# Performance work log

Hardware: AMD Instinct MI355X
Metric: run time of the kernel (lower is better)

## Reference

```python
import jax, jax.numpy as jnp
import numpy as np

jax.config.update("jax_enable_x64", True)  # int64 quantized math requires x64

Q = 23  # q23 fixed-point fraction bits


def _shift_linear(x, w, shift):
    """int64 GEMM with per-tensor arithmetic-shift rescale: (x @ w.T) >> shift.
    Models int64_bmm_broadcast with x_rescale=weight_rescale=1, res_rescale=shift
    (quotient part; the remainder is only used for the zk proof, not the output)."""
    acc = jnp.einsum('td,fd->tf', x, w.astype(jnp.int64))  # [T, out]
    return jnp.right_shift(acc, shift)  # arithmetic shift on signed int64


def silu_q23(r):
    """Fixed-point SiLU: s = round(silu(r / 2^Q) * 2^Q), int64 in/out."""
    xf = r.astype(jnp.float64) / float(1 << Q)
    y = xf * jax.nn.sigmoid(xf)
    return jnp.round(y * float(1 << Q)).astype(jnp.int64)


def setup_inputs() -> dict:
    key = jax.random.key(0)
    k1, k2, k3, k4 = jax.random.split(key, 4)
    T, D, F = 8192, 2048, 1408  # tokens, dim, inter_dim
    # q23 activations, centered so silu exercises both branches
    x = jax.random.randint(k1, (T, D), 0, 1 << 20, dtype=jnp.int64) - (1 << 19)
    w1 = (jax.random.randint(k2, (F, D), 0, 256, dtype=jnp.int32) - 128)
    w3 = (jax.random.randint(k3, (F, D), 0, 256, dtype=jnp.int32) - 128)
    w2 = (jax.random.randint(k4, (D, F), 0, 256, dtype=jnp.int32) - 128)
    return {"x": x, "w1": w1, "w2": w2, "w3": w3,
            "scale1": 23, "scale2": 23, "scale3": 23}


def reference(x, w1, w2, w3, scale1, scale2, scale3):
    # r1 = w1(x):  int64 GEMM + shift rescale
    r1 = _shift_linear(x, w1, scale1)            # [T, F] q23
    s1 = silu_q23(r1)                            # [T, F] q23
    r2 = _shift_linear(x, w3, scale3)            # [T, F] q23
    gate = jnp.right_shift(s1 * r2, Q)           # q23 * q23 >> 23 -> q23
    q = _shift_linear(gate, w2, scale2)          # [T, D]
    return q
```

## Files before the change

### kernel.cpp

```cpp
#include <hip/hip_runtime.h>
#include <math.h>

typedef int i32x4 __attribute__((ext_vector_type(4)));
typedef int i32x16 __attribute__((ext_vector_type(16)));

#define NT_M 128
#define NT_D 32
#define NT_F 22
#define DDIM 2048
#define FDIM 1408

#define OFFSWZ(r, k) (((r) << 6) + ((((((k) >> 4)) + ((r) >> 1)) & 3) << 4) + ((k) & 15))

__device__ __forceinline__ void gld_lds16(const void* gp, void* lp) {
  auto* l = reinterpret_cast<unsigned int __attribute__((address_space(3)))*>(
      (unsigned int)(unsigned long long)(lp));
  const auto* g = reinterpret_cast<const unsigned int __attribute__((address_space(1)))*>(
      (unsigned long long)(gp));
  __builtin_amdgcn_global_load_lds(g, l, 16, 0, 0);
}

__device__ __forceinline__ i32x16 zero16() {
  i32x16 z;
#pragma unroll
  for (int e = 0; e < 16; ++e) z[e] = 0;
  return z;
}

__global__ __launch_bounds__(256) void pack_x_kernel(const int* __restrict__ x,
                                                     signed char* __restrict__ XD) {
  const int tk = blockIdx.x;
  const int tm = blockIdx.y;
  const int tid = threadIdx.x;
  signed char* tile = XD + (size_t)(tm * NT_D + tk) * 3 * 4096;
  const int* base = x + (size_t)tm * 64 * DDIM + tk * 64;
#pragma unroll
  for (int i = 0; i < 4; ++i) {
    const int gi = i * 256 + tid;
    const int row = gi >> 4;
    const int k4 = (gi & 15) << 2;
    const i32x4 v = *(const i32x4*)(base + (size_t)row * DDIM + k4);
    unsigned p0 = 0, p1 = 0, p2 = 0;
#pragma unroll
    for (int j = 0; j < 4; ++j) {
      const int val = v[j];
      const int b0 = (int)(signed char)(val & 0xff);
      const int c = (val - b0) >> 8;
      const int b1 = (int)(signed char)(c & 0xff);
      const int b2 = (c - b1) >> 8;
      p0 |= ((unsigned)(val & 0xff)) << (8 * j);
      p1 |= ((unsigned)(c & 0xff)) << (8 * j);
      p2 |= ((unsigned)(b2 & 0xff)) << (8 * j);
    }
    const int off = OFFSWZ(row, k4);
    *(unsigned*)(tile + off) = p0;
    *(unsigned*)(tile + 4096 + off) = p1;
    *(unsigned*)(tile + 8192 + off) = p2;
  }
}

__global__ __launch_bounds__(256) void pack_w_kernel(const int* __restrict__ w1,
                                                     const int* __restrict__ w3,
                                                     const int* __restrict__ w2,
                                                     signed char* __restrict__ W1T,
                                                     signed char* __restrict__ W3T,
                                                     signed char* __restrict__ W2T) {
  const int which = blockIdx.y;
  const int t = blockIdx.x;
  const int tid = threadIdx.x;
  const int* src;
  signed char* dst;
  int rowstride, nk;
  if (which == 0)      { src = w1; dst = W1T; rowstride = DDIM; nk = NT_D; }
  else if (which == 1) { src = w3; dst = W3T; rowstride = DDIM; nk = NT_D; }
  else                 { src = w2; dst = W2T; rowstride = FDIM; nk = NT_F; }
  const int tr = t / nk, tk = t % nk;
  signed char* tile = dst + (size_t)t * 4096;
  const int* base = src + (size_t)tr * 64 * rowstride + tk * 64;
#pragma unroll
  for (int i = 0; i < 4; ++i) {
    const int gi = i * 256 + tid;
    const int row = gi >> 4;
    const int k4 = (gi & 15) << 2;
    const i32x4 v = *(const i32x4*)(base + (size_t)row * rowstride + k4);
    const unsigned p = ((unsigned)(v[0] & 0xff)) | ((unsigned)(v[1] & 0xff) << 8) |
                       ((unsigned)(v[2] & 0xff) << 16) | ((unsigned)(v[3] & 0xff) << 24);
    *(unsigned*)(tile + OFFSWZ(row, k4)) = p;
  }
}

__global__ __launch_bounds__(256, 2) void gemm1_kernel(
    const signed char* __restrict__ XD, const signed char* __restrict__ W1T,
    const signed char* __restrict__ W3T, signed char* __restrict__ GATE,
    const int* __restrict__ scale1p, const int* __restrict__ scale3p) {
  __shared__ __align__(16) signed char lds[40960];
  const int tid = threadIdx.x;
  const int wv = tid >> 6;
  const int lane = tid & 63;
  const int r32 = lane & 31;
  const int g = lane >> 5;
  const int tf = blockIdx.x;
  const int tm = blockIdx.y;
  const int wm = wv >> 1, wn = wv & 1;

  i32x16 acc10 = zero16(), acc11 = zero16(), acc12 = zero16();
  i32x16 acc30 = zero16(), acc31 = zero16(), acc32 = zero16();

  const signed char* srcAbase = XD + (size_t)tm * NT_D * 3 * 4096;
  const signed char* srcB1base = W1T + (size_t)tf * NT_D * 4096;
  const signed char* srcB3base = W3T + (size_t)tf * NT_D * 4096;

  auto stage = [&](int kt, int b) {
#pragma unroll
    for (int j = 0; j < 3; ++j) {
      const int ch = wv * 3 + j;
      gld_lds16(srcAbase + (size_t)kt * 12288 + ch * 1024 + lane * 16,
                lds + b * 12288 + ch * 1024);
    }
#pragma unroll
    for (int j = 0; j < 2; ++j) {
      const int ch = wv * 2 + j;
      const signed char* s = (ch < 4) ? srcB1base + (size_t)kt * 4096 + ch * 1024
                                      : srcB3base + (size_t)kt * 4096 + (ch - 4) * 1024;
      gld_lds16(s + lane * 16, lds + 24576 + b * 8192 + ch * 1024);
    }
  };

  stage(0, 0);

  const int arow = wm * 32 + r32;
  const int brow = wn * 32 + r32;
  const int aoffbase = arow * 64;
  const int boffbase = brow * 64;
  const int ash = arow >> 1;
  const int bsh = brow >> 1;

  for (int kt = 0; kt < NT_D; ++kt) {
    const int b = kt & 1;
    __syncthreads();
    if (kt + 1 < NT_D) stage(kt + 1, b ^ 1);
    const signed char* A = lds + b * 12288;
    const signed char* B = lds + 24576 + b * 8192;
#pragma unroll
    for (int kk = 0; kk < 2; ++kk) {
      const int ks = kk * 2 + g;
      const int sa = (ks + ash) & 3;
      const int sb = (ks + bsh) & 3;
      const i32x4 a0 = *(const i32x4*)(A + aoffbase + sa * 16);
      const i32x4 a1 = *(const i32x4*)(A + 4096 + aoffbase + sa * 16);
      const i32x4 a2 = *(const i32x4*)(A + 8192 + aoffbase + sa * 16);
      const i32x4 bb1 = *(const i32x4*)(B + boffbase + sb * 16);
      const i32x4 bb3 = *(const i32x4*)(B + 4096 + boffbase + sb * 16);
      acc10 = __builtin_amdgcn_mfma_i32_32x32x32_i8(a0, bb1, acc10, 0, 0, 0);
      acc11 = __builtin_amdgcn_mfma_i32_32x32x32_i8(a1, bb1, acc11, 0, 0, 0);
      acc12 = __builtin_amdgcn_mfma_i32_32x32x32_i8(a2, bb1, acc12, 0, 0, 0);
      acc30 = __builtin_amdgcn_mfma_i32_32x32x32_i8(a0, bb3, acc30, 0, 0, 0);
      acc31 = __builtin_amdgcn_mfma_i32_32x32x32_i8(a1, bb3, acc31, 0, 0, 0);
      acc32 = __builtin_amdgcn_mfma_i32_32x32x32_i8(a2, bb3, acc32, 0, 0, 0);
    }
  }

  const int s1v = scale1p[0];
  const int s3v = scale3p[0];
  signed char* gt = GATE + (size_t)(tm * NT_F + tf) * 4096;
  const int colf = wn * 32 + r32;
  const double QINV = 1.0 / 8388608.0;
#pragma unroll
  for (int e = 0; e < 16; ++e) {
    const int rowe = (e & 3) + 8 * (e >> 2) + 4 * g;
    const int ml = wm * 32 + rowe;
    const long long av1 =
        (long long)acc10[e] + ((long long)acc11[e] << 8) + ((long long)acc12[e] << 16);
    const long long r1 = av1 >> s1v;
    const long long av3 =
        (long long)acc30[e] + ((long long)acc31[e] << 8) + ((long long)acc32[e] << 16);
    const long long r2 = av3 >> s3v;
    const double xf = (double)r1 * QINV;
    const double t = exp(-fabs(xf));
    const double sg = (xf >= 0.0) ? (1.0 / (1.0 + t)) : (t / (1.0 + t));
    const long long s1q = (long long)rint((double)r1 * sg);
    const long long gv = (s1q * r2) >> 23;
    gt[OFFSWZ(ml, colf)] = (signed char)gv;
  }
}

__global__ __launch_bounds__(256, 2) void gemm2_kernel(
    const signed char* __restrict__ GATE, const signed char* __restrict__ W2T,
    int* __restrict__ out, const int* __restrict__ scale2p) {
  __shared__ __align__(16) signed char lds[32768];
  const int tid = threadIdx.x;
  const int wv = tid >> 6;
  const int lane = tid & 63;
  const int r32 = lane & 31;
  const int g = lane >> 5;
  const int tn = blockIdx.x;
  const int tm = blockIdx.y;
  const int wm = wv >> 1, wn = wv & 1;

  i32x16 acc00 = zero16(), acc01 = zero16(), acc10 = zero16(), acc11 = zero16();

  auto stage = [&](int kt, int b) {
#pragma unroll
    for (int j = 0; j < 2; ++j) {
      const int ch = wv * 2 + j;
      gld_lds16(GATE + ((size_t)((tm * 2 + (ch >> 2)) * NT_F + kt)) * 4096 + (ch & 3) * 1024 +
                    lane * 16,
                lds + b * 8192 + ch * 1024);
    }
#pragma unroll
    for (int j = 0; j < 2; ++j) {
      const int ch = wv * 2 + j;
      gld_lds16(W2T + ((size_t)((tn * 2 + (ch >> 2)) * NT_F + kt)) * 4096 + (ch & 3) * 1024 +
                    lane * 16,
                lds + 16384 + b * 8192 + ch * 1024);
    }
  };

  stage(0, 0);
  const int r0 = r32, r1r = 32 + r32;
  const int s0b = r0 >> 1, s1b = r1r >> 1;

  for (int kt = 0; kt < NT_F; ++kt) {
    const int b = kt & 1;
    __syncthreads();
    if (kt + 1 < NT_F) stage(kt + 1, b ^ 1);
    const signed char* A = lds + b * 8192 + wm * 4096;
    const signed char* B = lds + 16384 + b * 8192 + wn * 4096;
#pragma unroll
    for (int kk = 0; kk < 2; ++kk) {
      const int ks = kk * 2 + g;
      const int sa0 = (ks + s0b) & 3;
      const int sa1 = (ks + s1b) & 3;
      const i32x4 a0 = *(const i32x4*)(A + r0 * 64 + sa0 * 16);
      const i32x4 a1 = *(const i32x4*)(A + r1r * 64 + sa1 * 16);
      const i32x4 b0 = *(const i32x4*)(B + r0 * 64 + sa0 * 16);
      const i32x4 b1 = *(const i32x4*)(B + r1r * 64 + sa1 * 16);
      acc00 = __builtin_amdgcn_mfma_i32_32x32x32_i8(a0, b0, acc00, 0, 0, 0);
      acc01 = __builtin_amdgcn_mfma_i32_32x32x32_i8(a0, b1, acc01, 0, 0, 0);
      acc10 = __builtin_amdgcn_mfma_i32_32x32x32_i8(a1, b0, acc10, 0, 0, 0);
      acc11 = __builtin_amdgcn_mfma_i32_32x32x32_i8(a1, b1, acc11, 0, 0, 0);
    }
  }

  const int s2v = scale2p[0];
  int* obase = out + (size_t)(tm * 128 + wm * 64) * DDIM + tn * 128 + wn * 64;
#pragma unroll
  for (int e = 0; e < 16; ++e) {
    const int rowe = (e & 3) + 8 * (e >> 2) + 4 * g;
    obase[(size_t)rowe * DDIM + r32] = acc00[e] >> s2v;
    obase[(size_t)rowe * DDIM + 32 + r32] = acc01[e] >> s2v;
    obase[(size_t)(rowe + 32) * DDIM + r32] = acc10[e] >> s2v;
    obase[(size_t)(rowe + 32) * DDIM + 32 + r32] = acc11[e] >> s2v;
  }
}

extern "C" void kernel_launch(void* const* d_in, const int* in_sizes, int n_in,
                              void* d_out, int out_size, void* d_ws, size_t ws_size,
                              hipStream_t stream) {
  if (n_in < 7) return;
  const int* x = (const int*)d_in[0];
  const int* w1 = (const int*)d_in[1];
  const int* w2 = (const int*)d_in[2];
  const int* w3 = (const int*)d_in[3];
  const int* s1 = (const int*)d_in[4];
  const int* s2 = (const int*)d_in[5];
  const int* s3 = (const int*)d_in[6];
  signed char* ws = (signed char*)d_ws;
  int* out = (int*)d_out;

  const size_t XD_OFF = 0;
  const size_t XD_SZ = (size_t)NT_M * NT_D * 3 * 4096;
  const size_t WT_SZ = (size_t)NT_F * NT_D * 4096;
  const size_t W1_OFF = XD_OFF + XD_SZ;
  const size_t W3_OFF = W1_OFF + WT_SZ;
  const size_t W2_OFF = W3_OFF + WT_SZ;
  const size_t GATE_OFF = W2_OFF + WT_SZ;
  const size_t GATE_SZ = (size_t)NT_M * NT_F * 4096;
  if (ws_size < GATE_OFF + GATE_SZ) return;

  pack_x_kernel<<<dim3(NT_D, NT_M), 256, 0, stream>>>(x, ws + XD_OFF);
  pack_w_kernel<<<dim3(704, 3), 256, 0, stream>>>(w1, w3, w2, ws + W1_OFF, ws + W3_OFF,
                                                  ws + W2_OFF);
  gemm1_kernel<<<dim3(NT_F, NT_M), 256, 0, stream>>>(ws + XD_OFF, ws + W1_OFF, ws + W3_OFF,
                                                     ws + GATE_OFF, s1, s3);
  gemm2_kernel<<<dim3(DDIM / 128, NT_M / 2), 256, 0, stream>>>(ws + GATE_OFF, ws + W2_OFF,
                                                               out, s2);
}
```

Baseline: 207.2 us.

## Enlarge gemm1 M-tile to 128 rows with 8 waves and remap block order

gemm1 now uses 512-thread blocks covering two 64-row M tiles, so each staged W1/W3 tile is reused across twice as many rows and B traffic is halved. LDS grows to 64KB per block. Both GEMMs also switch to a 1D grid with block index swizzling, grouping 8 M-tiles across the XCDs to improve L2 locality. The risks are lower occupancy from the larger LDS footprint and the launch_bounds(512,4) register pressure.

```diff
diff --git a/kernel.cpp b/kernel.cpp
--- a/kernel.cpp
+++ b/kernel.cpp
@@ -89,58 +89,63 @@
   }
 }
 
-__global__ __launch_bounds__(256, 2) void gemm1_kernel(
+__global__ __launch_bounds__(512, 4) void gemm1_kernel(
     const signed char* __restrict__ XD, const signed char* __restrict__ W1T,
     const signed char* __restrict__ W3T, signed char* __restrict__ GATE,
     const int* __restrict__ scale1p, const int* __restrict__ scale3p) {
-  __shared__ __align__(16) signed char lds[40960];
+  __shared__ __align__(16) signed char lds[65536];
   const int tid = threadIdx.x;
   const int wv = tid >> 6;
   const int lane = tid & 63;
   const int r32 = lane & 31;
   const int g = lane >> 5;
-  const int tf = blockIdx.x;
-  const int tm = blockIdx.y;
+  const int bi = blockIdx.x;
+  const int c = bi & 7;
+  const int q = bi >> 3;
+  const int tm2 = (q / 22) * 8 + c;
+  const int tf = q % 22;
   const int wm = wv >> 1, wn = wv & 1;
 
   i32x16 acc10 = zero16(), acc11 = zero16(), acc12 = zero16();
   i32x16 acc30 = zero16(), acc31 = zero16(), acc32 = zero16();
 
-  const signed char* srcAbase = XD + (size_t)tm * NT_D * 3 * 4096;
   const signed char* srcB1base = W1T + (size_t)tf * NT_D * 4096;
   const signed char* srcB3base = W3T + (size_t)tf * NT_D * 4096;
 
   auto stage = [&](int kt, int b) {
+    const int sub = wv >> 2;
 #pragma unroll
     for (int j = 0; j < 3; ++j) {
       const int ch = wv * 3 + j;
-      gld_lds16(srcAbase + (size_t)kt * 12288 + ch * 1024 + lane * 16,
-                lds + b * 12288 + ch * 1024);
-    }
-#pragma unroll
-    for (int j = 0; j < 2; ++j) {
-      const int ch = wv * 2 + j;
+      const int chs = ch - sub * 12;
+      gld_lds16(XD + (size_t)((tm2 * 2 + sub) * NT_D + kt) * 12288 + chs * 1024 + lane * 16,
+                lds + b * 24576 + ch * 1024);
+    }
+    {
+      const int ch = wv;
       const signed char* s = (ch < 4) ? srcB1base + (size_t)kt * 4096 + ch * 1024
                                       : srcB3base + (size_t)kt * 4096 + (ch - 4) * 1024;
-      gld_lds16(s + lane * 16, lds + 24576 + b * 8192 + ch * 1024);
+      gld_lds16(s + lane * 16, lds + 49152 + b * 8192 + ch * 1024);
     }
   };
 
   stage(0, 0);
 
-  const int arow = wm * 32 + r32;
+  const int arowg = wm * 32 + r32;
+  const int asub = arowg >> 6;
+  const int arow = arowg & 63;
+  const int aoffbase = asub * 12288 + arow * 64;
+  const int ash = arow >> 1;
   const int brow = wn * 32 + r32;
-  const int aoffbase = arow * 64;
   const int boffbase = brow * 64;
-  const int ash = arow >> 1;
   const int bsh = brow >> 1;
 
   for (int kt = 0; kt < NT_D; ++kt) {
     const int b = kt & 1;
     __syncthreads();
     if (kt + 1 < NT_D) stage(kt + 1, b ^ 1);
-    const signed char* A = lds + b * 12288;
-    const signed char* B = lds + 24576 + b * 8192;
+    const signed char* A = lds + b * 24576;
+    const signed char* B = lds + 49152 + b * 8192;
 #pragma unroll
     for (int kk = 0; kk < 2; ++kk) {
       const int ks = kk * 2 + g;
@@ -162,13 +167,15 @@
 
   const int s1v = scale1p[0];
   const int s3v = scale3p[0];
-  signed char* gt = GATE + (size_t)(tm * NT_F + tf) * 4096;
   const int colf = wn * 32 + r32;
   const double QINV = 1.0 / 8388608.0;
 #pragma unroll
   for (int e = 0; e < 16; ++e) {
     const int rowe = (e & 3) + 8 * (e >> 2) + 4 * g;
-    const int ml = wm * 32 + rowe;
+    const int mlg = wm * 32 + rowe;
+    const int tmo = tm2 * 2 + (mlg >> 6);
+    const int mrow = mlg & 63;
+    signed char* gt = GATE + (size_t)(tmo * NT_F + tf) * 4096;
     const long long av1 =
         (long long)acc10[e] + ((long long)acc11[e] << 8) + ((long long)acc12[e] << 16);
     const long long r1 = av1 >> s1v;
@@ -180,7 +187,7 @@
     const double sg = (xf >= 0.0) ? (1.0 / (1.0 + t)) : (t / (1.0 + t));
     const long long s1q = (long long)rint((double)r1 * sg);
     const long long gv = (s1q * r2) >> 23;
-    gt[OFFSWZ(ml, colf)] = (signed char)gv;
+    gt[OFFSWZ(mrow, colf)] = (signed char)gv;
   }
 }
 
@@ -193,8 +200,11 @@
   const int lane = tid & 63;
   const int r32 = lane & 31;
   const int g = lane >> 5;
-  const int tn = blockIdx.x;
-  const int tm = blockIdx.y;
+  const int bi = blockIdx.x;
+  const int c = bi & 7;
+  const int q = bi >> 3;
+  const int tm = (q >> 4) * 8 + c;
+  const int tn = q & 15;
   const int wm = wv >> 1, wn = wv & 1;
 
   i32x16 acc00 = zero16(), acc01 = zero16(), acc10 = zero16(), acc11 = zero16();
@@ -281,8 +291,7 @@
   pack_x_kernel<<<dim3(NT_D, NT_M), 256, 0, stream>>>(x, ws + XD_OFF);
   pack_w_kernel<<<dim3(704, 3), 256, 0, stream>>>(w1, w3, w2, ws + W1_OFF, ws + W3_OFF,
                                                   ws + W2_OFF);
-  gemm1_kernel<<<dim3(NT_F, NT_M), 256, 0, stream>>>(ws + XD_OFF, ws + W1_OFF, ws + W3_OFF,
-                                                     ws + GATE_OFF, s1, s3);
-  gemm2_kernel<<<dim3(DDIM / 128, NT_M / 2), 256, 0, stream>>>(ws + GATE_OFF, ws + W2_OFF,
-                                                               out, s2);
-}
+  gemm1_kernel<<<dim3(1408), 512, 0, stream>>>(ws + XD_OFF, ws + W1_OFF, ws + W3_OFF,
+                                               ws + GATE_OFF, s1, s3);
+  gemm2_kernel<<<dim3(1024), 256, 0, stream>>>(ws + GATE_OFF, ws + W2_OFF, out, s2);
+}
```

After: 304.1 us. 1.47x slower.
